# Performance work log

Hardware: AMD Instinct MI355X
Metric: run time of the kernel (lower is better)

The kernel has to match this reference:

```python
import jax, jax.numpy as jnp
import numpy as np

N = 16384
RANK = 10
IN_F = 64
OUT_F = 64


def setup_inputs() -> dict:
    key = jax.random.key(0)
    k1, k2, k3, k4, k5 = jax.random.split(key, 5)
    return {
        "x": jax.random.normal(k1, (N, IN_F), dtype=jnp.float32),
        "source_embed": jax.random.normal(k2, (N, RANK), dtype=jnp.float32),
        "target_embed": jax.random.normal(k3, (RANK, N), dtype=jnp.float32),
        "W": jax.random.normal(k4, (OUT_F, IN_F), dtype=jnp.float32) * 0.1,
        "b": jax.random.normal(k5, (OUT_F,), dtype=jnp.float32) * 0.1,
    }


def reference(x, source_embed, target_embed, W, b):
    # Learned adjacency: [N, N] = softmax(relu(source @ target), row-wise)
    scores = jax.nn.relu(source_embed @ target_embed)  # [N, N]
    adj = jax.nn.softmax(scores, axis=1)               # [N, N]
    # Graph conv then linear (torch Linear: x @ W.T + b)
    agg = adj @ x                                       # [N, IN_F]
    return agg @ W.T + b                                # [N, OUT_F]
```

## Files before the change

### kernel.cpp

```cpp
#include <hip/hip_runtime.h>


constexpr int N    = 16384;
constexpr int RANK = 10;
constexpr int F    = 64;
constexpr int NH   = N / 2;

typedef float f32x4 __attribute__((ext_vector_type(4)));
typedef short bf16x8 __attribute__((ext_vector_type(8)));

constexpr float LOG2E = 1.4426950408889634f;

static __device__ __forceinline__ float fexp2(float x) {
    float r;
    asm("v_exp_f32 %0, %1" : "=v"(r) : "v"(x));
    return r;
}
static __device__ __forceinline__ unsigned short bfbits(float f) {
    return __builtin_bit_cast(unsigned short, (__bf16)f);
}

__global__ __launch_bounds__(256)
void prep(const float* __restrict__ x, const float* __restrict__ W,
          const float* __restrict__ te,
          uint4* __restrict__ yfrag, uint4* __restrict__ tefrag,
          int js0, int jt0)
{
    const int tid  = threadIdx.x;
    const int lane = tid & 63;
    const int g = lane >> 4, il = lane & 15;

    if (blockIdx.x < 256) {
        __shared__ float xs[32][68];
        const int jl = blockIdx.x;
        const int js = js0 + jl;
#pragma unroll
        for (int i = 0; i < 2; ++i) {
            const int fi = tid * 2 + i;
            const int r = fi >> 4, c4 = fi & 15;
            const float4 v = *reinterpret_cast<const float4*>(x + (size_t)(js * 32 + r) * F + c4 * 4);
            *reinterpret_cast<float4*>(&xs[r][c4 * 4]) = v;
        }
        __syncthreads();
        const int t = tid >> 6;
        const int f = t * 16 + il;
        float y[8];
#pragma unroll
        for (int b = 0; b < 8; ++b) y[b] = 0.f;
        const float* wr = W + f * F;
#pragma unroll
        for (int k4 = 0; k4 < F / 4; ++k4) {
            const float4 wv = *reinterpret_cast<const float4*>(wr + 4 * k4);
#pragma unroll
            for (int b = 0; b < 8; ++b) {
                const int row = 16 * (b >> 2) + 4 * g + (b & 3);
                const float4 xv = *reinterpret_cast<const float4*>(&xs[row][4 * k4]);
                y[b] = fmaf(xv.x, wv.x, y[b]);
                y[b] = fmaf(xv.y, wv.y, y[b]);
                y[b] = fmaf(xv.z, wv.z, y[b]);
                y[b] = fmaf(xv.w, wv.w, y[b]);
            }
        }
        union { unsigned short us[8]; uint4 v; } pk;
#pragma unroll
        for (int b = 0; b < 8; ++b) pk.us[b] = bfbits(y[b]);
        yfrag[(jl * 4 + t) * 64 + lane] = pk.v;
    } else {
        const int lt = (blockIdx.x - 256) * 4 + (tid >> 6);
        const int jt = jt0 + lt;
        union { unsigned short us[8]; uint4 v; } pk;
#pragma unroll
        for (int b = 0; b < 8; ++b) {
            const int k = 8 * g + b;
            unsigned short o = 0;
            if (k < 30) {
                const int band = (k < 10) ? 0 : (k < 20 ? 1 : 2);
                const int r = k - band * 10;
                const float v = te[r * N + jt * 16 + il];
                const __bf16 hb = (__bf16)v;
                o = (band == 2) ? bfbits(v - (float)hb)
                                : __builtin_bit_cast(unsigned short, hb);
            }
            pk.us[b] = o;
        }
        tefrag[lt * 64 + lane] = pk.v;
    }
}

__global__ __launch_bounds__(512, 2)
void gcn_main(const float* __restrict__ se, const uint4* __restrict__ tefrag,
              const uint4* __restrict__ yfrag, const float* __restrict__ bias,
              float* __restrict__ out, float* __restrict__ lsum_self,
              const float* __restrict__ lsum_other, int phase) {
    const int tid  = threadIdx.x;
    const int lane = tid & 63;
    const int wave = tid >> 6;
    const int g = lane >> 4, il = lane & 15;
    const int rowbase = blockIdx.x << 6;

    bf16x8 sef[4];
#pragma unroll
    for (int rt = 0; rt < 4; ++rt) {
        union { unsigned short us[8]; bf16x8 v; } pk;
        const int row = rowbase + rt * 16 + il;
#pragma unroll
        for (int b = 0; b < 8; ++b) {
            const int k = 8 * g + b;
            unsigned short o = 0;
            if (k < 30) {
                const int band = (k < 10) ? 0 : (k < 20 ? 1 : 2);
                const int r = k - band * 10;
                const float a = se[row * RANK + r] * LOG2E;
                const __bf16 hb = (__bf16)a;
                o = (band == 1) ? bfbits(a - (float)hb)
                                : __builtin_bit_cast(unsigned short, hb);
            }
            pk.us[b] = o;
        }
        sef[rt] = pk.v;
    }

    union { unsigned short us[8]; bf16x8 v; } onesu;
#pragma unroll
    for (int b = 0; b < 8; ++b) onesu.us[b] = 0x3F80;
    const bf16x8 ones = onesu.v;

    f32x4 acc[4][4];
#pragma unroll
    for (int rt = 0; rt < 4; ++rt)
#pragma unroll
        for (int ft = 0; ft < 4; ++ft) acc[rt][ft] = f32x4{0.f, 0.f, 0.f, 0.f};
    f32x4 accL[4];
#pragma unroll
    for (int rt = 0; rt < 4; ++rt) accL[rt] = f32x4{0.f, 0.f, 0.f, 0.f};

    const uint4* tb = tefrag + (size_t)wave * 64 * 64 + lane;
    const uint4* yb = yfrag + (size_t)wave * 32 * 256 + lane;

    for (int s = 0; s < 32; ++s) {
        const uint4 ta0 = tb[0];
        const uint4 ta1 = tb[64];
        const uint4 y0 = yb[0];
        const uint4 y1 = yb[64];
        const uint4 y2 = yb[128];
        const uint4 y3 = yb[192];
        const f32x4 z = {0.f, 0.f, 0.f, 0.f};

#pragma unroll
        for (int rt = 0; rt < 4; ++rt) {
            const f32x4 sc0 = __builtin_amdgcn_mfma_f32_16x16x32_bf16(__builtin_bit_cast(bf16x8, ta0), sef[rt], z, 0, 0, 0);
            const f32x4 sc1 = __builtin_amdgcn_mfma_f32_16x16x32_bf16(__builtin_bit_cast(bf16x8, ta1), sef[rt], z, 0, 0, 0);

            union { __bf16 h[8]; bf16x8 v; } af;
#pragma unroll
            for (int q = 0; q < 4; ++q) {
                af.h[q]     = (__bf16)fexp2(fmaxf(sc0[q], 0.f));
                af.h[4 + q] = (__bf16)fexp2(fmaxf(sc1[q], 0.f));
            }

            acc[rt][0] = __builtin_amdgcn_mfma_f32_16x16x32_bf16(af.v, __builtin_bit_cast(bf16x8, y0), acc[rt][0], 0, 0, 0);
            acc[rt][1] = __builtin_amdgcn_mfma_f32_16x16x32_bf16(af.v, __builtin_bit_cast(bf16x8, y1), acc[rt][1], 0, 0, 0);
            acc[rt][2] = __builtin_amdgcn_mfma_f32_16x16x32_bf16(af.v, __builtin_bit_cast(bf16x8, y2), acc[rt][2], 0, 0, 0);
            acc[rt][3] = __builtin_amdgcn_mfma_f32_16x16x32_bf16(af.v, __builtin_bit_cast(bf16x8, y3), acc[rt][3], 0, 0, 0);
            accL[rt]   = __builtin_amdgcn_mfma_f32_16x16x32_bf16(af.v, ones, accL[rt], 0, 0, 0);
        }

        tb += 128;
        yb += 256;
    }

    __shared__ float s_acc[4][4096];
    __shared__ float s_l[8][64];

    if (il == 0) {
#pragma unroll
        for (int rt = 0; rt < 4; ++rt)
#pragma unroll
            for (int q = 0; q < 4; ++q) s_l[wave][rt * 16 + 4 * g + q] = accL[rt][q];
    }
    if (wave < 4) {
#pragma unroll
        for (int rt = 0; rt < 4; ++rt)
#pragma unroll
            for (int ft = 0; ft < 4; ++ft)
#pragma unroll
                for (int q = 0; q < 4; ++q)
                    s_acc[wave][(rt * 16 + 4 * g + q) * 64 + ft * 16 + il] = acc[rt][ft][q];
    }
    __syncthreads();
    if (wave >= 4) {
#pragma unroll
        for (int rt = 0; rt < 4; ++rt)
#pragma unroll
            for (int ft = 0; ft < 4; ++ft)
#pragma unroll
                for (int q = 0; q < 4; ++q)
                    s_acc[wave - 4][(rt * 16 + 4 * g + q) * 64 + ft * 16 + il] += acc[rt][ft][q];
    }
    __syncthreads();

    const int e    = tid << 3;
    const int row  = e >> 6;
    const int feat = e & 63;
    f32x4 v0 = {0.f, 0.f, 0.f, 0.f}, v1 = {0.f, 0.f, 0.f, 0.f};
#pragma unroll
    for (int w = 0; w < 4; ++w) {
        v0 = v0 + *reinterpret_cast<const f32x4*>(&s_acc[w][row * 64 + feat]);
        v1 = v1 + *reinterpret_cast<const f32x4*>(&s_acc[w][row * 64 + feat + 4]);
    }
    float ls = 0.f;
#pragma unroll
    for (int w = 0; w < 8; ++w) ls += s_l[w][row];

    const int orow = rowbase + row;
    float* op = out + (size_t)orow * F + feat;

    if (phase == 0) {
        if (feat == 0) lsum_self[orow] = ls;
        float4 o0, o1;
        o0.x = v0[0]; o0.y = v0[1]; o0.z = v0[2]; o0.w = v0[3];
        o1.x = v1[0]; o1.y = v1[1]; o1.z = v1[2]; o1.w = v1[3];
        *reinterpret_cast<float4*>(op)     = o0;
        *reinterpret_cast<float4*>(op + 4) = o1;
    } else {
        const float4 p0 = *reinterpret_cast<const float4*>(op);
        const float4 p1 = *reinterpret_cast<const float4*>(op + 4);
        const float inv = 1.f / (ls + lsum_other[orow]);
        const float4 b0 = *reinterpret_cast<const float4*>(bias + feat);
        const float4 b1 = *reinterpret_cast<const float4*>(bias + feat + 4);
        float4 o0, o1;
        o0.x = (v0[0] + p0.x) * inv + b0.x;
        o0.y = (v0[1] + p0.y) * inv + b0.y;
        o0.z = (v0[2] + p0.z) * inv + b0.z;
        o0.w = (v0[3] + p0.w) * inv + b0.w;
        o1.x = (v1[0] + p1.x) * inv + b1.x;
        o1.y = (v1[1] + p1.y) * inv + b1.y;
        o1.z = (v1[2] + p1.z) * inv + b1.z;
        o1.w = (v1[3] + p1.w) * inv + b1.w;
        *reinterpret_cast<float4*>(op)     = o0;
        *reinterpret_cast<float4*>(op + 4) = o1;
    }
}

extern "C" void kernel_launch(void* const* d_in, const int* in_sizes, int n_in,
                              void* d_out, int out_size, void* d_ws, size_t ws_size,
                              hipStream_t stream) {
    const float* x  = (const float*)d_in[0];
    const float* se = (const float*)d_in[1];
    const float* te = (const float*)d_in[2];
    const float* W  = (const float*)d_in[3];
    const float* b  = (const float*)d_in[4];
    float* out = (float*)d_out;

    uint4* tefrag = (uint4*)d_ws;
    uint4* yfrag  = (uint4*)((char*)d_ws + (512u << 10));
    float* lsumA  = (float*)((char*)d_ws + (1536u << 10));
    float* lsumB  = lsumA + N;

    prep<<<384, 256, 0, stream>>>(x, W, te, yfrag, tefrag, 0, 0);
    gcn_main<<<N / 64, 512, 0, stream>>>(se, tefrag, yfrag, b, out, lsumA, lsumB, 0);

    prep<<<384, 256, 0, stream>>>(x, W, te, yfrag, tefrag, NH / 32, NH / 16);
    gcn_main<<<N / 64, 512, 0, stream>>>(se, tefrag, yfrag, b, out, lsumB, lsumA, 1);
}
```

Before: 151.0 us.

## Fuse prep and main passes into one cooperative kernel with grid syncs

Replaces the four launches (prep/main per half) with a single cooperative kernel of 256 blocks that builds the fragment buffers for each half, grid-syncs, runs the MFMA loop, and grid-syncs again before reusing the buffers. Accumulators stay in registers across both halves, so the partial output and row-sum round trip through global memory disappears. The main loop also gains register double-buffering of the next fragment loads. It removes launch gaps and the intermediate global traffic, at the cost of grid-wide barriers and a cooperative launch that requires all 256 blocks to be co-resident. The prefetch in the last iteration reads one step past the end of each wave's slice.

```diff
diff --git a/kernel.cpp b/kernel.cpp
--- a/kernel.cpp
+++ b/kernel.cpp
@@ -1,10 +1,12 @@
 #include <hip/hip_runtime.h>
+#include <hip/hip_cooperative_groups.h>
+
+namespace cg = cooperative_groups;
 
 
 constexpr int N    = 16384;
 constexpr int RANK = 10;
 constexpr int F    = 64;
-constexpr int NH   = N / 2;
 
 typedef float f32x4 __attribute__((ext_vector_type(4)));
 typedef short bf16x8 __attribute__((ext_vector_type(8)));
@@ -20,83 +22,24 @@
     return __builtin_bit_cast(unsigned short, (__bf16)f);
 }
 
-__global__ __launch_bounds__(256)
-void prep(const float* __restrict__ x, const float* __restrict__ W,
-          const float* __restrict__ te,
-          uint4* __restrict__ yfrag, uint4* __restrict__ tefrag,
-          int js0, int jt0)
+__global__ __launch_bounds__(512, 2)
+void gcn_all(const float* __restrict__ x, const float* __restrict__ W,
+             const float* __restrict__ te, const float* __restrict__ se,
+             uint4* __restrict__ tefrag, uint4* __restrict__ yfrag,
+             const float* __restrict__ bias, float* __restrict__ out)
 {
-    const int tid  = threadIdx.x;
-    const int lane = tid & 63;
-    const int g = lane >> 4, il = lane & 15;
-
-    if (blockIdx.x < 256) {
-        __shared__ float xs[32][68];
-        const int jl = blockIdx.x;
-        const int js = js0 + jl;
-#pragma unroll
-        for (int i = 0; i < 2; ++i) {
-            const int fi = tid * 2 + i;
-            const int r = fi >> 4, c4 = fi & 15;
-            const float4 v = *reinterpret_cast<const float4*>(x + (size_t)(js * 32 + r) * F + c4 * 4);
-            *reinterpret_cast<float4*>(&xs[r][c4 * 4]) = v;
-        }
-        __syncthreads();
-        const int t = tid >> 6;
-        const int f = t * 16 + il;
-        float y[8];
-#pragma unroll
-        for (int b = 0; b < 8; ++b) y[b] = 0.f;
-        const float* wr = W + f * F;
-#pragma unroll
-        for (int k4 = 0; k4 < F / 4; ++k4) {
-            const float4 wv = *reinterpret_cast<const float4*>(wr + 4 * k4);
-#pragma unroll
-            for (int b = 0; b < 8; ++b) {
-                const int row = 16 * (b >> 2) + 4 * g + (b & 3);
-                const float4 xv = *reinterpret_cast<const float4*>(&xs[row][4 * k4]);
-                y[b] = fmaf(xv.x, wv.x, y[b]);
-                y[b] = fmaf(xv.y, wv.y, y[b]);
-                y[b] = fmaf(xv.z, wv.z, y[b]);
-                y[b] = fmaf(xv.w, wv.w, y[b]);
-            }
-        }
-        union { unsigned short us[8]; uint4 v; } pk;
-#pragma unroll
-        for (int b = 0; b < 8; ++b) pk.us[b] = bfbits(y[b]);
-        yfrag[(jl * 4 + t) * 64 + lane] = pk.v;
-    } else {
-        const int lt = (blockIdx.x - 256) * 4 + (tid >> 6);
-        const int jt = jt0 + lt;
-        union { unsigned short us[8]; uint4 v; } pk;
-#pragma unroll
-        for (int b = 0; b < 8; ++b) {
-            const int k = 8 * g + b;
-            unsigned short o = 0;
-            if (k < 30) {
-                const int band = (k < 10) ? 0 : (k < 20 ? 1 : 2);
-                const int r = k - band * 10;
-                const float v = te[r * N + jt * 16 + il];
-                const __bf16 hb = (__bf16)v;
-                o = (band == 2) ? bfbits(v - (float)hb)
-                                : __builtin_bit_cast(unsigned short, hb);
-            }
-            pk.us[b] = o;
-        }
-        tefrag[lt * 64 + lane] = pk.v;
-    }
-}
-
-__global__ __launch_bounds__(512, 2)
-void gcn_main(const float* __restrict__ se, const uint4* __restrict__ tefrag,
-              const uint4* __restrict__ yfrag, const float* __restrict__ bias,
-              float* __restrict__ out, float* __restrict__ lsum_self,
-              const float* __restrict__ lsum_other, int phase) {
+    cg::grid_group grid = cg::this_grid();
+
     const int tid  = threadIdx.x;
     const int lane = tid & 63;
     const int wave = tid >> 6;
     const int g = lane >> 4, il = lane & 15;
-    const int rowbase = blockIdx.x << 6;
+    const int blk = blockIdx.x;
+    const int rowbase = blk << 6;
+
+    __shared__ float xs[32][68];
+    __shared__ float s_acc[4][4096];
+    __shared__ float s_l[8][64];
 
     bf16x8 sef[4];
 #pragma unroll
@@ -134,43 +77,105 @@
 #pragma unroll
     for (int rt = 0; rt < 4; ++rt) accL[rt] = f32x4{0.f, 0.f, 0.f, 0.f};
 
-    const uint4* tb = tefrag + (size_t)wave * 64 * 64 + lane;
-    const uint4* yb = yfrag + (size_t)wave * 32 * 256 + lane;
-
-    for (int s = 0; s < 32; ++s) {
-        const uint4 ta0 = tb[0];
-        const uint4 ta1 = tb[64];
-        const uint4 y0 = yb[0];
-        const uint4 y1 = yb[64];
-        const uint4 y2 = yb[128];
-        const uint4 y3 = yb[192];
-        const f32x4 z = {0.f, 0.f, 0.f, 0.f};
-
-#pragma unroll
-        for (int rt = 0; rt < 4; ++rt) {
-            const f32x4 sc0 = __builtin_amdgcn_mfma_f32_16x16x32_bf16(__builtin_bit_cast(bf16x8, ta0), sef[rt], z, 0, 0, 0);
-            const f32x4 sc1 = __builtin_amdgcn_mfma_f32_16x16x32_bf16(__builtin_bit_cast(bf16x8, ta1), sef[rt], z, 0, 0, 0);
-
-            union { __bf16 h[8]; bf16x8 v; } af;
-#pragma unroll
-            for (int q = 0; q < 4; ++q) {
-                af.h[q]     = (__bf16)fexp2(fmaxf(sc0[q], 0.f));
-                af.h[4 + q] = (__bf16)fexp2(fmaxf(sc1[q], 0.f));
-            }
-
-            acc[rt][0] = __builtin_amdgcn_mfma_f32_16x16x32_bf16(af.v, __builtin_bit_cast(bf16x8, y0), acc[rt][0], 0, 0, 0);
-            acc[rt][1] = __builtin_amdgcn_mfma_f32_16x16x32_bf16(af.v, __builtin_bit_cast(bf16x8, y1), acc[rt][1], 0, 0, 0);
-            acc[rt][2] = __builtin_amdgcn_mfma_f32_16x16x32_bf16(af.v, __builtin_bit_cast(bf16x8, y2), acc[rt][2], 0, 0, 0);
-            acc[rt][3] = __builtin_amdgcn_mfma_f32_16x16x32_bf16(af.v, __builtin_bit_cast(bf16x8, y3), acc[rt][3], 0, 0, 0);
-            accL[rt]   = __builtin_amdgcn_mfma_f32_16x16x32_bf16(af.v, ones, accL[rt], 0, 0, 0);
-        }
-
-        tb += 128;
-        yb += 256;
-    }
-
-    __shared__ float s_acc[4][4096];
-    __shared__ float s_l[8][64];
+    for (int half = 0; half < 2; ++half) {
+        if (tid < 256) {
+            const int js = (half << 8) + blk;
+#pragma unroll
+            for (int i = 0; i < 2; ++i) {
+                const int fi = tid * 2 + i;
+                const int r = fi >> 4, c4 = fi & 15;
+                const float4 v = *reinterpret_cast<const float4*>(
+                    x + (size_t)(js * 32 + r) * F + c4 * 4);
+                *reinterpret_cast<float4*>(&xs[r][c4 * 4]) = v;
+            }
+        }
+        __syncthreads();
+        if (tid < 256) {
+            const int t = tid >> 6;
+            const int f = t * 16 + il;
+            float y[8];
+#pragma unroll
+            for (int b = 0; b < 8; ++b) y[b] = 0.f;
+            const float* wr = W + f * F;
+#pragma unroll
+            for (int k4 = 0; k4 < F / 4; ++k4) {
+                const float4 wv = *reinterpret_cast<const float4*>(wr + 4 * k4);
+#pragma unroll
+                for (int b = 0; b < 8; ++b) {
+                    const int row = 16 * (b >> 2) + 4 * g + (b & 3);
+                    const float4 xv = *reinterpret_cast<const float4*>(&xs[row][4 * k4]);
+                    y[b] = fmaf(xv.x, wv.x, y[b]);
+                    y[b] = fmaf(xv.y, wv.y, y[b]);
+                    y[b] = fmaf(xv.z, wv.z, y[b]);
+                    y[b] = fmaf(xv.w, wv.w, y[b]);
+                }
+            }
+            union { unsigned short us[8]; uint4 v; } pk;
+#pragma unroll
+            for (int b = 0; b < 8; ++b) pk.us[b] = bfbits(y[b]);
+            yfrag[(blk * 4 + t) * 64 + lane] = pk.v;
+        } else if (tid < 384) {
+            const int lt = 2 * blk + ((tid - 256) >> 6);
+            const int jt = (half << 9) + lt;
+            union { unsigned short us[8]; uint4 v; } pk;
+#pragma unroll
+            for (int b = 0; b < 8; ++b) {
+                const int k = 8 * g + b;
+                unsigned short o = 0;
+                if (k < 30) {
+                    const int band = (k < 10) ? 0 : (k < 20 ? 1 : 2);
+                    const int r = k - band * 10;
+                    const float v = te[r * N + jt * 16 + il];
+                    const __bf16 hb = (__bf16)v;
+                    o = (band == 2) ? bfbits(v - (float)hb)
+                                    : __builtin_bit_cast(unsigned short, hb);
+                }
+                pk.us[b] = o;
+            }
+            tefrag[lt * 64 + lane] = pk.v;
+        }
+        grid.sync();
+
+        const uint4* tb = tefrag + (size_t)wave * 64 * 64 + lane;
+        const uint4* yb = yfrag  + (size_t)wave * 32 * 256 + lane;
+
+        uint4 ta0 = tb[0], ta1 = tb[64];
+        uint4 y0 = yb[0], y1 = yb[64], y2 = yb[128], y3 = yb[192];
+
+        for (int s = 0; s < 32; ++s) {
+            const uint4 nta0 = tb[128], nta1 = tb[192];
+            const uint4 ny0 = yb[256], ny1 = yb[320], ny2 = yb[384], ny3 = yb[448];
+
+            const f32x4 z = {0.f, 0.f, 0.f, 0.f};
+#pragma unroll
+            for (int rt = 0; rt < 4; ++rt) {
+                const f32x4 sc0 = __builtin_amdgcn_mfma_f32_16x16x32_bf16(
+                    __builtin_bit_cast(bf16x8, ta0), sef[rt], z, 0, 0, 0);
+                const f32x4 sc1 = __builtin_amdgcn_mfma_f32_16x16x32_bf16(
+                    __builtin_bit_cast(bf16x8, ta1), sef[rt], z, 0, 0, 0);
+
+                union { __bf16 h[8]; bf16x8 v; } af;
+#pragma unroll
+                for (int q = 0; q < 4; ++q) {
+                    af.h[q]     = (__bf16)fexp2(fmaxf(sc0[q], 0.f));
+                    af.h[4 + q] = (__bf16)fexp2(fmaxf(sc1[q], 0.f));
+                }
+
+                acc[rt][0] = __builtin_amdgcn_mfma_f32_16x16x32_bf16(af.v, __builtin_bit_cast(bf16x8, y0), acc[rt][0], 0, 0, 0);
+                acc[rt][1] = __builtin_amdgcn_mfma_f32_16x16x32_bf16(af.v, __builtin_bit_cast(bf16x8, y1), acc[rt][1], 0, 0, 0);
+                acc[rt][2] = __builtin_amdgcn_mfma_f32_16x16x32_bf16(af.v, __builtin_bit_cast(bf16x8, y2), acc[rt][2], 0, 0, 0);
+                acc[rt][3] = __builtin_amdgcn_mfma_f32_16x16x32_bf16(af.v, __builtin_bit_cast(bf16x8, y3), acc[rt][3], 0, 0, 0);
+                accL[rt]   = __builtin_amdgcn_mfma_f32_16x16x32_bf16(af.v, ones, accL[rt], 0, 0, 0);
+            }
+
+            ta0 = nta0; ta1 = nta1;
+            y0 = ny0; y1 = ny1; y2 = ny2; y3 = ny3;
+            tb += 128;
+            yb += 256;
+        }
+
+        if (half == 0) grid.sync();
+    }
 
     if (il == 0) {
 #pragma unroll
@@ -211,35 +216,22 @@
     float ls = 0.f;
 #pragma unroll
     for (int w = 0; w < 8; ++w) ls += s_l[w][row];
-
-    const int orow = rowbase + row;
-    float* op = out + (size_t)orow * F + feat;
-
-    if (phase == 0) {
-        if (feat == 0) lsum_self[orow] = ls;
-        float4 o0, o1;
-        o0.x = v0[0]; o0.y = v0[1]; o0.z = v0[2]; o0.w = v0[3];
-        o1.x = v1[0]; o1.y = v1[1]; o1.z = v1[2]; o1.w = v1[3];
-        *reinterpret_cast<float4*>(op)     = o0;
-        *reinterpret_cast<float4*>(op + 4) = o1;
-    } else {
-        const float4 p0 = *reinterpret_cast<const float4*>(op);
-        const float4 p1 = *reinterpret_cast<const float4*>(op + 4);
-        const float inv = 1.f / (ls + lsum_other[orow]);
-        const float4 b0 = *reinterpret_cast<const float4*>(bias + feat);
-        const float4 b1 = *reinterpret_cast<const float4*>(bias + feat + 4);
-        float4 o0, o1;
-        o0.x = (v0[0] + p0.x) * inv + b0.x;
-        o0.y = (v0[1] + p0.y) * inv + b0.y;
-        o0.z = (v0[2] + p0.z) * inv + b0.z;
-        o0.w = (v0[3] + p0.w) * inv + b0.w;
-        o1.x = (v1[0] + p1.x) * inv + b1.x;
-        o1.y = (v1[1] + p1.y) * inv + b1.y;
-        o1.z = (v1[2] + p1.z) * inv + b1.z;
-        o1.w = (v1[3] + p1.w) * inv + b1.w;
-        *reinterpret_cast<float4*>(op)     = o0;
-        *reinterpret_cast<float4*>(op + 4) = o1;
-    }
+    const float inv = 1.f / ls;
+
+    const float4 b0 = *reinterpret_cast<const float4*>(bias + feat);
+    const float4 b1 = *reinterpret_cast<const float4*>(bias + feat + 4);
+    float4 o0, o1;
+    o0.x = v0[0] * inv + b0.x;
+    o0.y = v0[1] * inv + b0.y;
+    o0.z = v0[2] * inv + b0.z;
+    o0.w = v0[3] * inv + b0.w;
+    o1.x = v1[0] * inv + b1.x;
+    o1.y = v1[1] * inv + b1.y;
+    o1.z = v1[2] * inv + b1.z;
+    o1.w = v1[3] * inv + b1.w;
+    float* op = out + (size_t)(rowbase + row) * F + feat;
+    *reinterpret_cast<float4*>(op)     = o0;
+    *reinterpret_cast<float4*>(op + 4) = o1;
 }
 
 extern "C" void kernel_launch(void* const* d_in, const int* in_sizes, int n_in,
@@ -254,12 +246,9 @@
 
     uint4* tefrag = (uint4*)d_ws;
     uint4* yfrag  = (uint4*)((char*)d_ws + (512u << 10));
-    float* lsumA  = (float*)((char*)d_ws + (1536u << 10));
-    float* lsumB  = lsumA + N;
-
-    prep<<<384, 256, 0, stream>>>(x, W, te, yfrag, tefrag, 0, 0);
-    gcn_main<<<N / 64, 512, 0, stream>>>(se, tefrag, yfrag, b, out, lsumA, lsumB, 0);
-
-    prep<<<384, 256, 0, stream>>>(x, W, te, yfrag, tefrag, NH / 32, NH / 16);
-    gcn_main<<<N / 64, 512, 0, stream>>>(se, tefrag, yfrag, b, out, lsumB, lsumA, 1);
-}
+
+    void* args[] = { (void*)&x, (void*)&W, (void*)&te, (void*)&se,
+                     (void*)&tefrag, (void*)&yfrag, (void*)&b, (void*)&out };
+    hipLaunchCooperativeKernel(reinterpret_cast<void*>(gcn_all),
+                               dim3(256), dim3(512), args, 0, stream);
+}
```

New measurement: 262.9 us. 1.74x slower.

## Double-buffer per-wave operand fragments in LDS via async global-to-LDS loads

Applied to the files above, without the earlier changes.

Replaces direct global register loads of the te and y fragments in the main loop with asynchronous global_load_lds copies into a per-wave double-buffered LDS staging area. The next iteration's fragments are prefetched while the current one is computed, hiding global memory latency behind the MFMA and exp work. The staging buffer is aliased with the reduction scratch, which adds a barrier before the epilogue. The extra LDS round trip and the hand-written waitcnt logic may cost cycles or be fragile.

```diff
diff --git a/kernel.cpp b/kernel.cpp
--- a/kernel.cpp
+++ b/kernel.cpp
@@ -18,6 +18,11 @@
 }
 static __device__ __forceinline__ unsigned short bfbits(float f) {
     return __builtin_bit_cast(unsigned short, (__bf16)f);
+}
+static __device__ __forceinline__ void load_lds16(const uint4* g, uint4* l) {
+    __builtin_amdgcn_global_load_lds(
+        (const __attribute__((address_space(1))) uint32_t*)g,
+        (__attribute__((address_space(3))) uint32_t*)l, 16, 0, 0);
 }
 
 __global__ __launch_bounds__(256)
@@ -98,6 +103,11 @@
     const int g = lane >> 4, il = lane & 15;
     const int rowbase = blockIdx.x << 6;
 
+    __shared__ alignas(16) char smem[8 * 2 * 6 * 64 * 16];
+    uint4 (*stage)[2][6][64] = reinterpret_cast<uint4 (*)[2][6][64]>(smem);
+    float (*s_acc)[4096]     = reinterpret_cast<float (*)[4096]>(smem);
+    __shared__ float s_l[8][64];
+
     bf16x8 sef[4];
 #pragma unroll
     for (int rt = 0; rt < 4; ++rt) {
@@ -135,21 +145,46 @@
     for (int rt = 0; rt < 4; ++rt) accL[rt] = f32x4{0.f, 0.f, 0.f, 0.f};
 
     const uint4* tb = tefrag + (size_t)wave * 64 * 64 + lane;
-    const uint4* yb = yfrag + (size_t)wave * 32 * 256 + lane;
+    const uint4* yb = yfrag  + (size_t)wave * 32 * 256 + lane;
+
+    load_lds16(tb,       &stage[wave][0][0][0]);
+    load_lds16(tb + 64,  &stage[wave][0][1][0]);
+    load_lds16(yb,       &stage[wave][0][2][0]);
+    load_lds16(yb + 64,  &stage[wave][0][3][0]);
+    load_lds16(yb + 128, &stage[wave][0][4][0]);
+    load_lds16(yb + 192, &stage[wave][0][5][0]);
 
     for (int s = 0; s < 32; ++s) {
-        const uint4 ta0 = tb[0];
-        const uint4 ta1 = tb[64];
-        const uint4 y0 = yb[0];
-        const uint4 y1 = yb[64];
-        const uint4 y2 = yb[128];
-        const uint4 y3 = yb[192];
+        const int buf = s & 1;
+        if (s < 31) {
+            asm volatile("s_waitcnt lgkmcnt(0)" ::: "memory");
+            const uint4* tn = tb + (size_t)(s + 1) * 128;
+            const uint4* yn = yb + (size_t)(s + 1) * 256;
+            load_lds16(tn,       &stage[wave][buf ^ 1][0][0]);
+            load_lds16(tn + 64,  &stage[wave][buf ^ 1][1][0]);
+            load_lds16(yn,       &stage[wave][buf ^ 1][2][0]);
+            load_lds16(yn + 64,  &stage[wave][buf ^ 1][3][0]);
+            load_lds16(yn + 128, &stage[wave][buf ^ 1][4][0]);
+            load_lds16(yn + 192, &stage[wave][buf ^ 1][5][0]);
+            asm volatile("s_waitcnt vmcnt(6)" ::: "memory");
+        } else {
+            asm volatile("s_waitcnt vmcnt(0)" ::: "memory");
+        }
+
+        const uint4 ta0 = stage[wave][buf][0][lane];
+        const uint4 ta1 = stage[wave][buf][1][lane];
+        const uint4 y0  = stage[wave][buf][2][lane];
+        const uint4 y1  = stage[wave][buf][3][lane];
+        const uint4 y2  = stage[wave][buf][4][lane];
+        const uint4 y3  = stage[wave][buf][5][lane];
         const f32x4 z = {0.f, 0.f, 0.f, 0.f};
 
 #pragma unroll
         for (int rt = 0; rt < 4; ++rt) {
-            const f32x4 sc0 = __builtin_amdgcn_mfma_f32_16x16x32_bf16(__builtin_bit_cast(bf16x8, ta0), sef[rt], z, 0, 0, 0);
-            const f32x4 sc1 = __builtin_amdgcn_mfma_f32_16x16x32_bf16(__builtin_bit_cast(bf16x8, ta1), sef[rt], z, 0, 0, 0);
+            const f32x4 sc0 = __builtin_amdgcn_mfma_f32_16x16x32_bf16(
+                __builtin_bit_cast(bf16x8, ta0), sef[rt], z, 0, 0, 0);
+            const f32x4 sc1 = __builtin_amdgcn_mfma_f32_16x16x32_bf16(
+                __builtin_bit_cast(bf16x8, ta1), sef[rt], z, 0, 0, 0);
 
             union { __bf16 h[8]; bf16x8 v; } af;
 #pragma unroll
@@ -164,13 +199,9 @@
             acc[rt][3] = __builtin_amdgcn_mfma_f32_16x16x32_bf16(af.v, __builtin_bit_cast(bf16x8, y3), acc[rt][3], 0, 0, 0);
             accL[rt]   = __builtin_amdgcn_mfma_f32_16x16x32_bf16(af.v, ones, accL[rt], 0, 0, 0);
         }
-
-        tb += 128;
-        yb += 256;
-    }
-
-    __shared__ float s_acc[4][4096];
-    __shared__ float s_l[8][64];
+    }
+
+    __syncthreads();
 
     if (il == 0) {
 #pragma unroll
```

New measurement: 159.2 us. 5.5% more time.
